# Kernel optimization log

Hardware: AMD Instinct MI355X
Metric: run time of the kernel (lower is better)

## Reference

```python
import jax, jax.numpy as jnp
import numpy as np

B, L, S, D, H = 4, 1024, 1024, 1024, 16
HD = D // H  # head_dim = 64


def setup_inputs() -> dict:
    key = jax.random.key(0)
    ks = jax.random.split(key, 12)
    s = 1.0 / np.sqrt(D)
    return {
        "query": jax.random.normal(ks[0], (B, L, D), jnp.float32),
        "key": jax.random.normal(ks[1], (B, S, D), jnp.float32),
        "value": jax.random.normal(ks[2], (B, S, D), jnp.float32),
        "key_padding_mask": jax.random.randint(ks[3], (B, S), 0, 2) > 0,
        "Wq": jax.random.normal(ks[4], (D, D), jnp.float32) * s,
        "bq": jnp.zeros((D,), jnp.float32),
        "Wk": jax.random.normal(ks[5], (D, D), jnp.float32) * s,
        "bk": jnp.zeros((D,), jnp.float32),
        "Wv": jax.random.normal(ks[6], (D, D), jnp.float32) * s,
        "bv": jnp.zeros((D,), jnp.float32),
        "Wo": jax.random.normal(ks[7], (D, D), jnp.float32) * s,
        "bo": jnp.zeros((D,), jnp.float32),
    }


def reference(query, key, value, key_padding_mask, Wq, bq, Wk, bk, Wv, bv, Wo, bo):
    bs, tgt, _ = query.shape
    src = key.shape[1]
    # Q/K/V projections (nn.Linear: x @ W.T + b)
    q = query @ Wq.T + bq
    k = key @ Wk.T + bk
    v = value @ Wv.T + bv
    # split heads: (B, T, H, HD)
    q = q.reshape(bs, tgt, H, HD)
    k = k.reshape(bs, src, H, HD)
    v = v.reshape(bs, src, H, HD)
    # scaled dot-product attention with key padding mask (True = masked)
    scale = 1.0 / jnp.sqrt(jnp.asarray(HD, q.dtype))
    scores = jnp.einsum("blhd,bshd->bhls", q, k) * scale  # (B,H,L,S)
    neg_inf = jnp.asarray(-jnp.inf, scores.dtype)
    scores = scores + jnp.where(key_padding_mask[:, None, None, :], neg_inf, 0.0)
    attn = jax.nn.softmax(scores, axis=-1)
    out = jnp.einsum("bhls,bshd->blhd", attn, v).reshape(bs, tgt, D)
    return out @ Wo.T + bo
```

## Files before the change

kernel.cpp:

```cpp
#include <hip/hip_runtime.h>
#include <hip/hip_bf16.h>


typedef __bf16 bf16;
typedef __bf16 bf16x4 __attribute__((ext_vector_type(4)));
typedef __bf16 bf16x8 __attribute__((ext_vector_type(8)));
typedef float floatx4 __attribute__((ext_vector_type(4)));

#define D_MODEL 1024
#define NHEAD   16
#define HDIM    64
#define BATCH   4
#define SEQ     1024
#define M_ROWS  (BATCH * SEQ)
#define ACT_N   ((size_t)M_ROWS * D_MODEL)
#define W_N     ((size_t)D_MODEL * D_MODEL)
#define SC2     0.18033688011112042f

#define GLD(gp, lp) __builtin_amdgcn_global_load_lds( \
    (__attribute__((address_space(1))) void*)(gp), \
    (__attribute__((address_space(3))) void*)(lp), 16, 0, 0)

__global__ __launch_bounds__(256)
void k_convert_all(const float* __restrict__ a0, const float* __restrict__ a1,
                   const float* __restrict__ a2,
                   const float* __restrict__ w0, const float* __restrict__ w1,
                   const float* __restrict__ w2, const float* __restrict__ w3,
                   bf16* __restrict__ dst,
                   const unsigned* __restrict__ m, float* __restrict__ mbias)
{
    if (blockIdx.x == 8192) {
        __shared__ unsigned viol[4];
        __shared__ int fmsh;
        if (threadIdx.x < 4) viol[threadIdx.x] = 0;
        __syncthreads();
        unsigned a = 0, b = 0, c = 0, d = 0;
        for (int i = threadIdx.x; i < 1024; i += 256) {
            unsigned v = m[i];
            if (v > 1u) a = 1;
            if (((v & 0xFFu) > 1u) || (((v >> 8) & 0xFFu) > 1u) ||
                (((v >> 16) & 0xFFu) > 1u) || (((v >> 24) & 0xFFu) > 1u)) b = 1;
            unsigned lo = v & 0xFFFFu, hi = v >> 16;
            if (!((lo == 0u || lo == 0x3F80u) && (hi == 0u || hi == 0x3F80u))) c = 1;
            if (lo != 0u) d = 1;
        }
        if (a) atomicOr(&viol[0], 1u);
        if (b) atomicOr(&viol[1], 1u);
        if (c) atomicOr(&viol[2], 1u);
        if (d) atomicOr(&viol[3], 1u);
        __syncthreads();
        if (threadIdx.x == 0) {
            int fm;
            if (!viol[0])      fm = 1;
            else if (!viol[1]) fm = 0;
            else if (!viol[2]) fm = viol[3] ? 2 : 3;
            else               fm = 0;
            fmsh = fm;
        }
        __syncthreads();
        const int fm = fmsh;
        for (int i = 0; i < 16; ++i) {
            int s = i * 256 + threadIdx.x;
            bool msk;
            if (fm == 1)      msk = ((const int*)m)[s] != 0;
            else if (fm == 2) msk = ((const unsigned short*)m)[s] != 0;
            else if (fm == 3) msk = ((const unsigned*)m)[s] != 0;
            else              msk = ((const unsigned char*)m)[s] != 0;
            mbias[s] = msk ? -1e30f : 0.f;
        }
        return;
    }

    size_t i = ((size_t)blockIdx.x * 256 + threadIdx.x) * 8;
    const float* src; size_t off;
    if (i < ((size_t)12 << 20)) {
        int z = (int)(i >> 22);
        src = (z == 0) ? a0 : (z == 1) ? a1 : a2;
        off = i & (((size_t)1 << 22) - 1);
    } else {
        size_t r = i - ((size_t)12 << 20);
        int j = (int)(r >> 20);
        src = (j == 0) ? w0 : (j == 1) ? w1 : (j == 2) ? w2 : w3;
        off = r & (((size_t)1 << 20) - 1);
    }
    float4 f0 = ((const float4*)(src + off))[0];
    float4 f1 = ((const float4*)(src + off))[1];
    bf16x8 o;
    o[0] = (bf16)f0.x; o[1] = (bf16)f0.y; o[2] = (bf16)f0.z; o[3] = (bf16)f0.w;
    o[4] = (bf16)f1.x; o[5] = (bf16)f1.y; o[6] = (bf16)f1.z; o[7] = (bf16)f1.w;
    *(bf16x8*)(dst + i) = o;
}

template<typename CT, int NT>
__device__ __forceinline__ void gemm8_core(const bf16* __restrict__ A,
                                           const bf16* __restrict__ W,
                                           const float* __restrict__ bias,
                                           CT* __restrict__ C,
                                           int m0, int n0, bool rowBias,
                                           bf16* __restrict__ As0,
                                           bf16* __restrict__ Bs0)
{
    const int t    = threadIdx.x;
    const int lane = t & 63;
    const int w    = t >> 6;
    const int wm   = w >> 2;
    const int wn   = w & 3;
    const int l15  = lane & 15;
    const int quad = lane >> 4;
    const int lx   = l15 & 7;

    constexpr int NJ = NT / 128;
    constexpr int BSTRIDE = NT * 64;

    floatx4 acc[8][NT / 64] = {};

    int srow[2], schk[2], ldso[2];
    #pragma unroll
    for (int j = 0; j < 2; ++j) {
        int i = j * 512 + t;
        srow[j] = i >> 3;
        schk[j] = (i & 7) ^ (srow[j] & 7);
        ldso[j] = (j * 512 + w * 64) * 8;
    }

    #define STAGE_HALF(src, rb, k0s, h, dstbuf) do {                          \
        _Pragma("unroll")                                                     \
        for (int j = 0; j < 2; ++j)                                           \
            GLD((src) + (size_t)((rb) + (h) * 128 + srow[j]) * D_MODEL        \
                    + (k0s) + schk[j] * 8,                                    \
                (dstbuf) + (h) * 8192 + ldso[j]);                             \
    } while (0)

    STAGE_HALF(A, m0, 0, 0, As0);
    STAGE_HALF(A, m0, 0, 1, As0);
    STAGE_HALF(W, n0, 0, 0, Bs0);
    if constexpr (NT == 256) STAGE_HALF(W, n0, 0, 1, Bs0);
    __syncthreads();

    for (int kt = 0; kt < 16; ++kt) {
        const int nk = (kt + 1) * 64;
        const bf16* __restrict__ Ab = As0 + (kt & 1) * 16384;
        const bf16* __restrict__ Bb = Bs0 + (kt & 1) * BSTRIDE;
        bf16* __restrict__ An = As0 + ((kt + 1) & 1) * 16384;
        bf16* __restrict__ Bn = Bs0 + ((kt + 1) & 1) * BSTRIDE;

        #pragma unroll
        for (int ph = 0; ph < 4; ++ph) {
            const int mq = ph >> 1, nq = ph & 1;

            if (nk < D_MODEL) {
                if constexpr (NT == 256) {
                    if (ph == 0)      STAGE_HALF(A, m0, nk, 0, An);
                    else if (ph == 1) STAGE_HALF(A, m0, nk, 1, An);
                    else if (ph == 2) STAGE_HALF(W, n0, nk, 0, Bn);
                    else              STAGE_HALF(W, n0, nk, 1, Bn);
                } else {
                    if (ph == 0)      STAGE_HALF(A, m0, nk, 0, An);
                    else if (ph == 1) STAGE_HALF(A, m0, nk, 1, An);
                    else if (ph == 2) STAGE_HALF(W, n0, nk, 0, Bn);
                }
            }

            bf16x8 af[4][2], bfr[NJ][2];
            #pragma unroll
            for (int ii = 0; ii < 4; ++ii) {
                int row = wm * 128 + mq * 64 + ii * 16 + l15;
                #pragma unroll
                for (int kk = 0; kk < 2; ++kk)
                    af[ii][kk] = *(const bf16x8*)
                        &Ab[row * 64 + (((kk * 4 + quad) ^ lx)) * 8];
            }
            #pragma unroll
            for (int jj = 0; jj < NJ; ++jj) {
                int row = wn * (NT / 4) + nq * (NT / 8) + jj * 16 + l15;
                #pragma unroll
                for (int kk = 0; kk < 2; ++kk)
                    bfr[jj][kk] = *(const bf16x8*)
                        &Bb[row * 64 + (((kk * 4 + quad) ^ lx)) * 8];
            }

            #pragma unroll
            for (int ii = 0; ii < 4; ++ii)
                #pragma unroll
                for (int jj = 0; jj < NJ; ++jj)
                    #pragma unroll
                    for (int kk = 0; kk < 2; ++kk)
                        acc[mq * 4 + ii][nq * NJ + jj] =
                            __builtin_amdgcn_mfma_f32_16x16x32_bf16(
                                af[ii][kk], bfr[jj][kk],
                                acc[mq * 4 + ii][nq * NJ + jj], 0, 0, 0);
        }
        __syncthreads();
    }

    #pragma unroll
    for (int i = 0; i < 8; ++i) {
        int rowb = m0 + wm * 128 + i * 16 + quad * 4;
        float bvr[4];
        if (rowBias) {
            #pragma unroll
            for (int r = 0; r < 4; ++r) bvr[r] = bias[rowb + r];
        }
        #pragma unroll
        for (int jf = 0; jf < NT / 64; ++jf) {
            int col = n0 + wn * (NT / 4) + jf * 16 + l15;
            float bc = rowBias ? 0.f : bias[col];
            #pragma unroll
            for (int r = 0; r < 4; ++r) {
                float val = acc[i][jf][r] + (rowBias ? bvr[r] : bc);
                C[(size_t)(rowb + r) * D_MODEL + col] = (CT)val;
            }
        }
    }
    #undef STAGE_HALF
}

__global__ __launch_bounds__(512, 2)
void k_gemm_proj(const bf16* __restrict__ cq, const bf16* __restrict__ ck,
                 const bf16* __restrict__ cv,
                 const bf16* __restrict__ cWq, const bf16* __restrict__ cWk,
                 const bf16* __restrict__ cWv,
                 const float* __restrict__ bq, const float* __restrict__ bk,
                 const float* __restrict__ bv,
                 bf16* __restrict__ qproj, bf16* __restrict__ kproj,
                 bf16* __restrict__ vt)
{
    extern __shared__ __align__(16) bf16 smem[];
    bf16* As0 = smem;
    bf16* Bs0 = smem + 32768;

    const int bid = blockIdx.x;
    const int tid = (bid & 7) * 24 + (bid >> 3);
    if (tid < 64) {
        gemm8_core<bf16, 256>(cq, cWq, bq, qproj,
                              (tid >> 2) * 256, (tid & 3) * 256, false, As0, Bs0);
    } else if (tid < 128) {
        int u = tid - 64;
        gemm8_core<bf16, 256>(ck, cWk, bk, kproj,
                              (u >> 2) * 256, (u & 3) * 256, false, As0, Bs0);
    } else {
        int v = tid - 128;
        int b = v >> 4, m = (v >> 2) & 3, n = v & 3;
        gemm8_core<bf16, 256>(cWv, cv + (size_t)b * W_N, bv,
                              vt + (size_t)b * W_N, m * 256, n * 256, true,
                              As0, Bs0);
    }
}

__global__ __launch_bounds__(512, 2)
void k_gemm_o(const bf16* __restrict__ A, const bf16* __restrict__ W,
              const float* __restrict__ bb, float* __restrict__ C)
{
    extern __shared__ __align__(16) bf16 smem[];
    bf16* As0 = smem;
    bf16* Bs0 = smem + 32768;

    const int bid = blockIdx.x;
    const int tid = (bid & 7) * 16 + (bid >> 3);
    gemm8_core<float, 128>(A, W, bb, C, (tid >> 3) * 256, (tid & 7) * 128,
                           false, As0, Bs0);
}

__global__ __launch_bounds__(256)
void k_attn(const bf16* __restrict__ qproj, const bf16* __restrict__ kproj,
            const bf16* __restrict__ vt, const float* __restrict__ mbias_g,
            bf16* __restrict__ ctx)
{
    __shared__ alignas(16) bf16 Kst[2][4096];
    __shared__ alignas(16) bf16 Vst[2][4096];
    __shared__ alignas(16) bf16 Past[8192];

    const int t    = threadIdx.x;
    const int lane = t & 63;
    const int w    = t >> 6;
    const int l15  = lane & 15;
    const int quad = lane >> 4;

    const int b  = blockIdx.x >> 4;
    const int h  = blockIdx.x & 15;
    const int q0 = blockIdx.y * 128;

    #pragma unroll
    for (int i = 0; i < 2; ++i) {
        int f   = w * 2 + i;
        int row = (f >> 1) * 16 + l15;
        int cb  = (f & 1) * 32 + quad * 8;
        GLD(kproj + (size_t)(b * SEQ + row) * D_MODEL + h * HDIM + cb,
            Kst[0] + f * 512);
        GLD(vt + (size_t)(b * 1024 + h * HDIM + row) * D_MODEL + cb,
            Vst[0] + f * 512);
    }

    bf16x8 qf[2][2];
    #pragma unroll
    for (int g = 0; g < 2; ++g)
        #pragma unroll
        for (int kk = 0; kk < 2; ++kk)
            qf[g][kk] = *(const bf16x8*)(qproj
                + (size_t)(b * SEQ + q0 + w * 32 + g * 16 + l15) * D_MODEL
                + h * HDIM + kk * 32 + quad * 8);

    __syncthreads();

    bf16x8 ones;
    #pragma unroll
    for (int e = 0; e < 8; ++e) ones[e] = (bf16)1.0f;

    floatx4 o[2][4] = {};
    floatx4 accl[2] = {};

    const int rswz = lane ^ ((lane >> 3) & 7);
    const float* __restrict__ mbb = mbias_g + b * SEQ;

    int cur = 0;
    for (int s0 = 0; s0 < SEQ; s0 += 64) {
        if (s0 + 64 < SEQ) {
            #pragma unroll
            for (int i = 0; i < 2; ++i) {
                int f   = w * 2 + i;
                int row = (f >> 1) * 16 + l15;
                int cb  = (f & 1) * 32 + quad * 8;
                GLD(kproj + (size_t)(b * SEQ + s0 + 64 + row) * D_MODEL
                        + h * HDIM + cb,
                    Kst[cur ^ 1] + f * 512);
                GLD(vt + (size_t)(b * 1024 + h * HDIM + row) * D_MODEL
                        + s0 + 64 + cb,
                    Vst[cur ^ 1] + f * 512);
            }
        }

        floatx4 s_acc[2][4] = {};
        #pragma unroll
        for (int j = 0; j < 4; ++j) {
            bf16x8 kf0 = *(const bf16x8*)&Kst[cur][(j * 2 + 0) * 512 + lane * 8];
            bf16x8 kf1 = *(const bf16x8*)&Kst[cur][(j * 2 + 1) * 512 + lane * 8];
            #pragma unroll
            for (int g = 0; g < 2; ++g) {
                s_acc[g][j] = __builtin_amdgcn_mfma_f32_16x16x32_bf16(
                    kf0, qf[g][0], s_acc[g][j], 0, 0, 0);
                s_acc[g][j] = __builtin_amdgcn_mfma_f32_16x16x32_bf16(
                    kf1, qf[g][1], s_acc[g][j], 0, 0, 0);
            }
        }

        #pragma unroll
        for (int j = 0; j < 4; ++j) {
            float4 mb4 = *(const float4*)&mbb[s0 + j * 16 + quad * 4];
            int c = (j >> 1) * 64 + ((j & 1) * 2 + (quad >> 1)) * 16 + l15;
            int phys = c ^ ((c >> 3) & 7);
            #pragma unroll
            for (int g = 0; g < 2; ++g) {
                bf16x4 pk;
                pk[0] = (bf16)__builtin_amdgcn_exp2f(
                    fmaf(s_acc[g][j][0], SC2, mb4.x));
                pk[1] = (bf16)__builtin_amdgcn_exp2f(
                    fmaf(s_acc[g][j][1], SC2, mb4.y));
                pk[2] = (bf16)__builtin_amdgcn_exp2f(
                    fmaf(s_acc[g][j][2], SC2, mb4.z));
                pk[3] = (bf16)__builtin_amdgcn_exp2f(
                    fmaf(s_acc[g][j][3], SC2, mb4.w));
                *(bf16x4*)&Past[(w * 2 + g) * 1024 + phys * 8
                                + (quad & 1) * 4] = pk;
            }
        }
        __builtin_amdgcn_wave_barrier();

        bf16x8 pf[2][2];
        #pragma unroll
        for (int g = 0; g < 2; ++g)
            #pragma unroll
            for (int kk = 0; kk < 2; ++kk)
                pf[g][kk] = *(const bf16x8*)
                    &Past[(w * 2 + g) * 1024 + (kk * 64 + rswz) * 8];

        #pragma unroll
        for (int g = 0; g < 2; ++g)
            #pragma unroll
            for (int kk = 0; kk < 2; ++kk)
                accl[g] = __builtin_amdgcn_mfma_f32_16x16x32_bf16(
                    pf[g][kk], ones, accl[g], 0, 0, 0);

        #pragma unroll
        for (int j = 0; j < 4; ++j) {
            bf16x8 vf0 = *(const bf16x8*)&Vst[cur][(j * 2 + 0) * 512 + lane * 8];
            bf16x8 vf1 = *(const bf16x8*)&Vst[cur][(j * 2 + 1) * 512 + lane * 8];
            #pragma unroll
            for (int g = 0; g < 2; ++g) {
                o[g][j] = __builtin_amdgcn_mfma_f32_16x16x32_bf16(
                    pf[g][0], vf0, o[g][j], 0, 0, 0);
                o[g][j] = __builtin_amdgcn_mfma_f32_16x16x32_bf16(
                    pf[g][1], vf1, o[g][j], 0, 0, 0);
            }
        }

        __syncthreads();
        cur ^= 1;
    }

    #pragma unroll
    for (int g = 0; g < 2; ++g) {
        float inv[4];
        #pragma unroll
        for (int r = 0; r < 4; ++r)
            inv[r] = (accl[g][r] > 0.f) ? 1.f / accl[g][r] : 0.f;
        #pragma unroll
        for (int j = 0; j < 4; ++j)
            #pragma unroll
            for (int r = 0; r < 4; ++r) {
                int row = q0 + w * 32 + g * 16 + quad * 4 + r;
                int col = h * HDIM + j * 16 + l15;
                ctx[(size_t)(b * SEQ + row) * D_MODEL + col] =
                    (bf16)(o[g][j][r] * inv[r]);
            }
    }
}

extern "C" void kernel_launch(void* const* d_in, const int* in_sizes, int n_in,
                              void* d_out, int out_size, void* d_ws, size_t ws_size,
                              hipStream_t stream)
{
    char* wsb = (char*)d_ws;
    float* mbias = (float*)wsb;
    bf16* cbase = (bf16*)(wsb + 65536);
    bf16 *cq = cbase, *ck = cq + ACT_N, *cv = ck + ACT_N;
    bf16 *cWq = cv + ACT_N, *cWk = cWq + W_N, *cWv = cWk + W_N, *cWo = cWv + W_N;
    bf16* qproj = cWo + W_N;
    bf16* kproj = qproj + ACT_N;
    bf16* vt    = kproj + ACT_N;
    bf16* ctx   = vt + ACT_N;
    float* out  = (float*)d_out;

    static bool attrset = false;
    if (!attrset) {
        hipFuncSetAttribute((const void*)k_gemm_proj,
                            hipFuncAttributeMaxDynamicSharedMemorySize, 131072);
        hipFuncSetAttribute((const void*)k_gemm_o,
                            hipFuncAttributeMaxDynamicSharedMemorySize, 131072);
        attrset = true;
    }

    k_convert_all<<<8193, 256, 0, stream>>>(
        (const float*)d_in[0], (const float*)d_in[1], (const float*)d_in[2],
        (const float*)d_in[4], (const float*)d_in[6], (const float*)d_in[8],
        (const float*)d_in[10], cbase, (const unsigned*)d_in[3], mbias);

    k_gemm_proj<<<192, 512, 131072, stream>>>(cq, ck, cv, cWq, cWk, cWv,
                                              (const float*)d_in[5],
                                              (const float*)d_in[7],
                                              (const float*)d_in[9],
                                              qproj, kproj, vt);
    k_attn<<<dim3(64, 8), 256, 0, stream>>>(qproj, kproj, vt, mbias, ctx);
    k_gemm_o<<<128, 512, 98304, stream>>>(ctx, cWo, (const float*)d_in[11], out);
}
```

Before: 210.2 us.

## Software-pipeline attention loop: overlap previous tile's PV MFMAs with current QK

```diff
diff --git a/kernel.cpp b/kernel.cpp
--- a/kernel.cpp
+++ b/kernel.cpp
@@ -267,7 +267,7 @@
             bf16* __restrict__ ctx)
 {
     __shared__ alignas(16) bf16 Kst[2][4096];
-    __shared__ alignas(16) bf16 Vst[2][4096];
+    __shared__ alignas(16) bf16 Vst[3][4096];
     __shared__ alignas(16) bf16 Past[8192];
 
     const int t    = threadIdx.x;
@@ -280,16 +280,22 @@
     const int h  = blockIdx.x & 15;
     const int q0 = blockIdx.y * 128;
 
-    #pragma unroll
-    for (int i = 0; i < 2; ++i) {
-        int f   = w * 2 + i;
-        int row = (f >> 1) * 16 + l15;
-        int cb  = (f & 1) * 32 + quad * 8;
-        GLD(kproj + (size_t)(b * SEQ + row) * D_MODEL + h * HDIM + cb,
-            Kst[0] + f * 512);
-        GLD(vt + (size_t)(b * 1024 + h * HDIM + row) * D_MODEL + cb,
-            Vst[0] + f * 512);
-    }
+    #define STAGE_KV(s0s, kbuf, vbuf) do {                                    \
+        _Pragma("unroll")                                                     \
+        for (int i = 0; i < 2; ++i) {                                         \
+            int f   = w * 2 + i;                                              \
+            int row = (f >> 1) * 16 + l15;                                    \
+            int cb  = (f & 1) * 32 + quad * 8;                                \
+            GLD(kproj + (size_t)(b * SEQ + (s0s) + row) * D_MODEL             \
+                    + h * HDIM + cb,                                          \
+                Kst[kbuf] + f * 512);                                         \
+            GLD(vt + (size_t)(b * 1024 + h * HDIM + row) * D_MODEL            \
+                    + (s0s) + cb,                                             \
+                Vst[vbuf] + f * 512);                                         \
+        }                                                                     \
+    } while (0)
+
+    STAGE_KV(0, 0, 0);
 
     bf16x8 qf[2][2];
     #pragma unroll
@@ -308,25 +314,27 @@
 
     floatx4 o[2][4] = {};
     floatx4 accl[2] = {};
+    bf16x8 pf_prev[2][2];
 
     const int rswz = lane ^ ((lane >> 3) & 7);
     const float* __restrict__ mbb = mbias_g + b * SEQ;
 
     int cur = 0;
-    for (int s0 = 0; s0 < SEQ; s0 += 64) {
-        if (s0 + 64 < SEQ) {
-            #pragma unroll
-            for (int i = 0; i < 2; ++i) {
-                int f   = w * 2 + i;
-                int row = (f >> 1) * 16 + l15;
-                int cb  = (f & 1) * 32 + quad * 8;
-                GLD(kproj + (size_t)(b * SEQ + s0 + 64 + row) * D_MODEL
-                        + h * HDIM + cb,
-                    Kst[cur ^ 1] + f * 512);
-                GLD(vt + (size_t)(b * 1024 + h * HDIM + row) * D_MODEL
-                        + s0 + 64 + cb,
-                    Vst[cur ^ 1] + f * 512);
-            }
+    int vbp = 2, vb = 0, vbn = 1;
+
+    for (int ti = 0; ti < 16; ++ti) {
+        const int s0 = ti * 64;
+        if (ti < 15)
+            STAGE_KV(s0 + 64, cur ^ 1, vbn);
+
+        bf16x8 vfp[4][2];
+        if (ti > 0) {
+            #pragma unroll
+            for (int j = 0; j < 4; ++j)
+                #pragma unroll
+                for (int kk = 0; kk < 2; ++kk)
+                    vfp[j][kk] = *(const bf16x8*)
+                        &Vst[vbp][(j * 2 + kk) * 512 + lane * 8];
         }
 
         floatx4 s_acc[2][4] = {};
@@ -341,6 +349,24 @@
                 s_acc[g][j] = __builtin_amdgcn_mfma_f32_16x16x32_bf16(
                     kf1, qf[g][1], s_acc[g][j], 0, 0, 0);
             }
+        }
+
+        if (ti > 0) {
+            #pragma unroll
+            for (int g = 0; g < 2; ++g)
+                #pragma unroll
+                for (int kk = 0; kk < 2; ++kk)
+                    accl[g] = __builtin_amdgcn_mfma_f32_16x16x32_bf16(
+                        pf_prev[g][kk], ones, accl[g], 0, 0, 0);
+            #pragma unroll
+            for (int j = 0; j < 4; ++j)
+                #pragma unroll
+                for (int g = 0; g < 2; ++g) {
+                    o[g][j] = __builtin_amdgcn_mfma_f32_16x16x32_bf16(
+                        pf_prev[g][0], vfp[j][0], o[g][j], 0, 0, 0);
+                    o[g][j] = __builtin_amdgcn_mfma_f32_16x16x32_bf16(
+                        pf_prev[g][1], vfp[j][1], o[g][j], 0, 0, 0);
+                }
         }
 
         #pragma unroll
@@ -365,36 +391,41 @@
         }
         __builtin_amdgcn_wave_barrier();
 
-        bf16x8 pf[2][2];
         #pragma unroll
         for (int g = 0; g < 2; ++g)
             #pragma unroll
             for (int kk = 0; kk < 2; ++kk)
-                pf[g][kk] = *(const bf16x8*)
+                pf_prev[g][kk] = *(const bf16x8*)
                     &Past[(w * 2 + g) * 1024 + (kk * 64 + rswz) * 8];
 
+        __syncthreads();
+        cur ^= 1;
+        int tmp = vbp; vbp = vb; vb = vbn; vbn = tmp;
+    }
+
+    {
+        bf16x8 vfp[4][2];
+        #pragma unroll
+        for (int j = 0; j < 4; ++j)
+            #pragma unroll
+            for (int kk = 0; kk < 2; ++kk)
+                vfp[j][kk] = *(const bf16x8*)
+                    &Vst[vbp][(j * 2 + kk) * 512 + lane * 8];
         #pragma unroll
         for (int g = 0; g < 2; ++g)
             #pragma unroll
             for (int kk = 0; kk < 2; ++kk)
                 accl[g] = __builtin_amdgcn_mfma_f32_16x16x32_bf16(
-                    pf[g][kk], ones, accl[g], 0, 0, 0);
-
-        #pragma unroll
-        for (int j = 0; j < 4; ++j) {
-            bf16x8 vf0 = *(const bf16x8*)&Vst[cur][(j * 2 + 0) * 512 + lane * 8];
-            bf16x8 vf1 = *(const bf16x8*)&Vst[cur][(j * 2 + 1) * 512 + lane * 8];
+                    pf_prev[g][kk], ones, accl[g], 0, 0, 0);
+        #pragma unroll
+        for (int j = 0; j < 4; ++j)
             #pragma unroll
             for (int g = 0; g < 2; ++g) {
                 o[g][j] = __builtin_amdgcn_mfma_f32_16x16x32_bf16(
-                    pf[g][0], vf0, o[g][j], 0, 0, 0);
+                    pf_prev[g][0], vfp[j][0], o[g][j], 0, 0, 0);
                 o[g][j] = __builtin_amdgcn_mfma_f32_16x16x32_bf16(
-                    pf[g][1], vf1, o[g][j], 0, 0, 0);
-            }
-        }
-
-        __syncthreads();
-        cur ^= 1;
+                    pf_prev[g][1], vfp[j][1], o[g][j], 0, 0, 0);
+            }
     }
 
     #pragma unroll
@@ -413,6 +444,7 @@
                     (bf16)(o[g][j][r] * inv[r]);
             }
     }
+    #undef STAGE_KV
 }
 
 extern "C" void kernel_launch(void* const* d_in, const int* in_sizes, int n_in,
```

Measured after the change: 214.7 us. 2.1% more time.
